# Optimization experiments

Hardware: AMD Instinct MI355X
Metric: run time of the kernel (lower is better)

The kernel has to match this reference:

```python
import jax, jax.numpy as jnp
import numpy as np

IN_DIM, DIM_MSA, PAIR_DIM = 256, 32, 64
B, L = 1, 512


def setup_inputs() -> dict:
    key = jax.random.key(0)
    k0, k1, k2, k3, k4 = jax.random.split(key, 5)
    seq_rep = jax.random.normal(k0, (B, L, IN_DIM), dtype=jnp.float32)
    # torch nn.Linear params: weight [out, in], bias [out]
    s1 = 1.0 / np.sqrt(IN_DIM)
    W1 = jax.random.uniform(k1, (DIM_MSA, IN_DIM), jnp.float32, -s1, s1)
    b1 = jax.random.uniform(k2, (DIM_MSA,), jnp.float32, -s1, s1)
    s2 = 1.0 / np.sqrt(DIM_MSA * DIM_MSA)
    W2 = jax.random.uniform(k3, (PAIR_DIM, DIM_MSA * DIM_MSA), jnp.float32, -s2, s2)
    b2 = jax.random.uniform(k4, (PAIR_DIM,), jnp.float32, -s2, s2)
    return {"seq_rep": seq_rep, "W1": W1, "b1": b1, "W2": W2, "b2": b2}


def reference(seq_rep, W1, b1, W2, b2):
    # proj_down1: [B,L,in_dim] -> [B,L,dim_msa]
    x = seq_rep @ W1.T + b1
    # outer product: 'bid,bjc -> bijcd' then flatten (c d)
    # [B,L(i),L(j),c(dim_msa),d(dim_msa)]
    outer = jnp.einsum('bid,bjc->bijcd', x, x)
    Bb, Li, Lj = outer.shape[:3]
    outer = outer.reshape(Bb, Li, Lj, DIM_MSA * DIM_MSA)  # (c d), c-major
    # proj_down2: -> [B,L,L,pairwise_dim]
    return outer @ W2.T + b2
```

## Files before the change

### kernel.cpp

```cpp
#include <hip/hip_runtime.h>


static constexpr int LL  = 512;
static constexpr int IND = 256;
static constexpr int DM  = 32;
static constexpr int PD  = 64;

typedef _Float16 f16x8 __attribute__((ext_vector_type(8)));
typedef float    f32x16 __attribute__((ext_vector_type(16)));

#define LGKM_BARRIER() do { \
    asm volatile("s_waitcnt lgkmcnt(0)" ::: "memory"); \
    __builtin_amdgcn_s_barrier(); \
  } while (0)

__global__ __launch_bounds__(256) void k_proj1(const float* __restrict__ seq,
                                               const float* __restrict__ W1,
                                               const float* __restrict__ b1,
                                               float* __restrict__ xg,
                                               _Float16* __restrict__ xgh) {
  __shared__ float part[8][DM];
  const int i   = blockIdx.x;
  const int t   = threadIdx.x;
  const int d   = t & 31;
  const int seg = t >> 5;
  const float* srow = seq + (size_t)i * IND + seg * 32;
  const float* wrow = W1  + (size_t)d * IND + seg * 32;
  float acc = 0.f;
#pragma unroll
  for (int k = 0; k < 32; k += 4) {
    const float4 s4 = *(const float4*)(srow + k);
    const float4 w4 = *(const float4*)(wrow + k);
    acc = fmaf(s4.x, w4.x, acc);
    acc = fmaf(s4.y, w4.y, acc);
    acc = fmaf(s4.z, w4.z, acc);
    acc = fmaf(s4.w, w4.w, acc);
  }
  part[seg][d] = acc;
  __syncthreads();
  if (t < DM) {
    float s = b1[t];
#pragma unroll
    for (int g = 0; g < 8; ++g) s += part[g][t];
    xg[i * DM + t]  = s;
    xgh[i * DM + t] = (_Float16)s;
  }
}

__global__ __launch_bounds__(256) void k_y(const float* __restrict__ xg,
                                           const float* __restrict__ W2,
                                           _Float16* __restrict__ Ygh) {
  __shared__ __align__(16) float xs[64][36];
  __shared__ __align__(16) float ws2[64][36];
  const int c     = blockIdx.x & 31;
  const int ibase = (blockIdx.x >> 5) * 64;
  const int t     = threadIdx.x;
#pragma unroll
  for (int k = 0; k < 2; ++k) {
    const int idx = t + k * 256;
    const int il = idx >> 3, d4 = idx & 7;
    const float4 v = *(const float4*)(xg + (size_t)(ibase + il) * DM + d4 * 4);
    *(float4*)&xs[il][d4 * 4] = v;
  }
#pragma unroll
  for (int k = 0; k < 2; ++k) {
    const int idx = t + k * 256;
    const int p = idx >> 3, d4 = idx & 7;
    const float4 v = *(const float4*)(W2 + (size_t)p * (DM * DM) + c * DM + d4 * 4);
    *(float4*)&ws2[p][d4 * 4] = v;
  }
  __syncthreads();
  const int p  = t & 63;
  const int ig = t >> 6;
  float wv[DM];
#pragma unroll
  for (int q = 0; q < 8; ++q) {
    const float4 v = *(const float4*)&ws2[p][q * 4];
    wv[q * 4 + 0] = v.x; wv[q * 4 + 1] = v.y;
    wv[q * 4 + 2] = v.z; wv[q * 4 + 3] = v.w;
  }
#pragma unroll
  for (int il = 0; il < 16; ++il) {
    const int row = ig * 16 + il;
    float a = 0.f;
#pragma unroll
    for (int q = 0; q < 8; ++q) {
      const float4 v = *(const float4*)&xs[row][q * 4];
      a = fmaf(wv[q * 4 + 0], v.x, a);
      a = fmaf(wv[q * 4 + 1], v.y, a);
      a = fmaf(wv[q * 4 + 2], v.z, a);
      a = fmaf(wv[q * 4 + 3], v.w, a);
    }
    Ygh[((size_t)(ibase + row) * DM + c) * PD + p] = (_Float16)a;
  }
}

static constexpr int XPAD = 40;

__global__ __launch_bounds__(128, 3) void k_outer(const _Float16* __restrict__ xgh,
                                                  const _Float16* __restrict__ Ygh,
                                                  const float* __restrict__ b2,
                                                  float* __restrict__ out) {
  __shared__ __align__(16) _Float16 xbs[128 * XPAD];
  __shared__ __align__(16) _Float16 ybs[2 * DM * PD];
  __shared__ __align__(16) float    obuf[2][32 * 32];
  const int q  = blockIdx.x & 3;
  const int i0 = blockIdx.x >> 2;
  const int t  = threadIdx.x;

  const int lane = t & 63;
  const int w    = t >> 6;
  const int l31  = lane & 31;
  const int lh   = lane >> 5;
  const int pn   = w * 32 + l31;
  float* const obufW = &obuf[w][0];
  const float4 bias4 = *(const float4*)(b2 + w * 32 + (lane & 7) * 4);

  {
    const f16x8* src = (const f16x8*)(xgh + (size_t)(q * 128 + t) * DM);
    _Float16* dst = &xbs[t * XPAD];
    *(f16x8*)(dst)      = src[0];
    *(f16x8*)(dst + 8)  = src[1];
    *(f16x8*)(dst + 16) = src[2];
    *(f16x8*)(dst + 24) = src[3];
  }
  {
    const f16x8* ys = (const f16x8*)(Ygh + (size_t)i0 * (DM * PD));
    *(f16x8*)&ybs[t * 8]        = ys[t];
    *(f16x8*)&ybs[1024 + t * 8] = ys[128 + t];
  }
  LGKM_BARRIER();

  const f16x8* ys1 = (const f16x8*)(Ygh + (size_t)(i0 + 256) * (DM * PD));
  const f16x8 n0 = ys1[t];
  const f16x8 n1 = ys1[128 + t];

  auto process = [&](int i, const _Float16* __restrict__ yb) {
    f16x8 b0, b1;
#pragma unroll
    for (int e = 0; e < 8; ++e) {
      b0[e] = yb[(lh * 8 + e) * PD + pn];
      b1[e] = yb[(16 + lh * 8 + e) * PD + pn];
    }
    const size_t orow0 = ((size_t)i * LL + q * 128) * PD;
#pragma unroll
    for (int jt = 0; jt < 4; ++jt) {
      const int ai = (jt * 32 + l31) * XPAD + lh * 8;
      const f16x8 a0 = *(const f16x8*)&xbs[ai];
      const f16x8 a1 = *(const f16x8*)&xbs[ai + 16];
      f32x16 acc = {};
      acc = __builtin_amdgcn_mfma_f32_32x32x16_f16(a0, b0, acc, 0, 0, 0);
      acc = __builtin_amdgcn_mfma_f32_32x32x16_f16(a1, b1, acc, 0, 0, 0);
#pragma unroll
      for (int r = 0; r < 16; ++r) {
        const int row = (r & 3) + 8 * (r >> 2) + 4 * lh;
        obufW[row * 32 + l31] = acc[r];
      }
#pragma unroll
      for (int k = 0; k < 4; ++k) {
        const int idx = lane + k * 64;
        const int row = idx >> 3, pseg = idx & 7;
        float4 v = *(const float4*)&obufW[idx * 4];
        v.x += bias4.x; v.y += bias4.y; v.z += bias4.z; v.w += bias4.w;
        *(float4*)(out + orow0 + (size_t)(jt * 32 + row) * PD + w * 32 + pseg * 4) = v;
      }
    }
  };

  process(i0, ybs);

  *(f16x8*)&ybs[2048 + t * 8]        = n0;
  *(f16x8*)&ybs[2048 + 1024 + t * 8] = n1;
  LGKM_BARRIER();

  process(i0 + 256, ybs + 2048);
}

extern "C" void kernel_launch(void* const* d_in, const int* in_sizes, int n_in,
                              void* d_out, int out_size, void* d_ws, size_t ws_size,
                              hipStream_t stream) {
  const float* seq = (const float*)d_in[0];
  const float* W1  = (const float*)d_in[1];
  const float* b1  = (const float*)d_in[2];
  const float* W2  = (const float*)d_in[3];
  const float* b2  = (const float*)d_in[4];
  float* out = (float*)d_out;

  float* xg     = (float*)d_ws;
  _Float16* xgh = (_Float16*)(xg + LL * DM);
  _Float16* Ygh = (_Float16*)(xg + LL * DM + LL * DM / 2);

  k_proj1<<<LL, 256, 0, stream>>>(seq, W1, b1, xg, xgh);
  k_y<<<256, 256, 0, stream>>>(xg, W2, Ygh);
  k_outer<<<LL * 2, 128, 0, stream>>>(xgh, Ygh, b2, out);
}
```

Measured before the change: 27.36 us.

## Fuse proj1 into Y kernel, computing x via fp16 MFMA per block

New measurement: 30.25 us. +10.5%, slower.

```diff
diff --git a/kernel.cpp b/kernel.cpp
--- a/kernel.cpp
+++ b/kernel.cpp
@@ -14,54 +14,29 @@
     __builtin_amdgcn_s_barrier(); \
   } while (0)
 
-__global__ __launch_bounds__(256) void k_proj1(const float* __restrict__ seq,
+__device__ __forceinline__ f16x8 cvt8(const float* __restrict__ p) {
+  const float4 a = *(const float4*)p;
+  const float4 b = *(const float4*)(p + 4);
+  f16x8 r;
+  r[0] = (_Float16)a.x; r[1] = (_Float16)a.y;
+  r[2] = (_Float16)a.z; r[3] = (_Float16)a.w;
+  r[4] = (_Float16)b.x; r[5] = (_Float16)b.y;
+  r[6] = (_Float16)b.z; r[7] = (_Float16)b.w;
+  return r;
+}
+
+__global__ __launch_bounds__(256) void k_front(const float* __restrict__ seq,
                                                const float* __restrict__ W1,
                                                const float* __restrict__ b1,
-                                               float* __restrict__ xg,
-                                               _Float16* __restrict__ xgh) {
-  __shared__ float part[8][DM];
-  const int i   = blockIdx.x;
-  const int t   = threadIdx.x;
-  const int d   = t & 31;
-  const int seg = t >> 5;
-  const float* srow = seq + (size_t)i * IND + seg * 32;
-  const float* wrow = W1  + (size_t)d * IND + seg * 32;
-  float acc = 0.f;
-#pragma unroll
-  for (int k = 0; k < 32; k += 4) {
-    const float4 s4 = *(const float4*)(srow + k);
-    const float4 w4 = *(const float4*)(wrow + k);
-    acc = fmaf(s4.x, w4.x, acc);
-    acc = fmaf(s4.y, w4.y, acc);
-    acc = fmaf(s4.z, w4.z, acc);
-    acc = fmaf(s4.w, w4.w, acc);
-  }
-  part[seg][d] = acc;
-  __syncthreads();
-  if (t < DM) {
-    float s = b1[t];
-#pragma unroll
-    for (int g = 0; g < 8; ++g) s += part[g][t];
-    xg[i * DM + t]  = s;
-    xgh[i * DM + t] = (_Float16)s;
-  }
-}
-
-__global__ __launch_bounds__(256) void k_y(const float* __restrict__ xg,
-                                           const float* __restrict__ W2,
-                                           _Float16* __restrict__ Ygh) {
+                                               const float* __restrict__ W2,
+                                               _Float16* __restrict__ xgh,
+                                               _Float16* __restrict__ Ygh) {
   __shared__ __align__(16) float xs[64][36];
   __shared__ __align__(16) float ws2[64][36];
   const int c     = blockIdx.x & 31;
   const int ibase = (blockIdx.x >> 5) * 64;
   const int t     = threadIdx.x;
-#pragma unroll
-  for (int k = 0; k < 2; ++k) {
-    const int idx = t + k * 256;
-    const int il = idx >> 3, d4 = idx & 7;
-    const float4 v = *(const float4*)(xg + (size_t)(ibase + il) * DM + d4 * 4);
-    *(float4*)&xs[il][d4 * 4] = v;
-  }
+
 #pragma unroll
   for (int k = 0; k < 2; ++k) {
     const int idx = t + k * 256;
@@ -69,29 +44,54 @@
     const float4 v = *(const float4*)(W2 + (size_t)p * (DM * DM) + c * DM + d4 * 4);
     *(float4*)&ws2[p][d4 * 4] = v;
   }
+
+  const int w = t >> 6, lane = t & 63, l31 = lane & 31, lh = lane >> 5;
+  if (w < 2) {
+    const int mbase = ibase + w * 32;
+    const float* arow = seq + (size_t)(mbase + l31) * IND + lh * 8;
+    const float* brow = W1  + (size_t)l31 * IND + lh * 8;
+    const float bias1 = b1[l31];
+    f32x16 acc = {};
+#pragma unroll
+    for (int ks = 0; ks < 16; ++ks) {
+      const f16x8 af = cvt8(arow + ks * 16);
+      const f16x8 bf = cvt8(brow + ks * 16);
+      acc = __builtin_amdgcn_mfma_f32_32x32x16_f16(af, bf, acc, 0, 0, 0);
+    }
+#pragma unroll
+    for (int r = 0; r < 16; ++r) {
+      const int mrow = (r & 3) + 8 * (r >> 2) + 4 * lh;
+      const float v = acc[r] + bias1;
+      xs[w * 32 + mrow][l31] = v;
+      if (c == 0) xgh[(size_t)(mbase + mrow) * DM + l31] = (_Float16)v;
+    }
+  }
   __syncthreads();
-  const int p  = t & 63;
-  const int ig = t >> 6;
-  float wv[DM];
-#pragma unroll
-  for (int q = 0; q < 8; ++q) {
-    const float4 v = *(const float4*)&ws2[p][q * 4];
-    wv[q * 4 + 0] = v.x; wv[q * 4 + 1] = v.y;
-    wv[q * 4 + 2] = v.z; wv[q * 4 + 3] = v.w;
-  }
-#pragma unroll
-  for (int il = 0; il < 16; ++il) {
-    const int row = ig * 16 + il;
-    float a = 0.f;
+
+  {
+    const int p  = t & 63;
+    const int ig = t >> 6;
+    float wv[DM];
 #pragma unroll
     for (int q = 0; q < 8; ++q) {
-      const float4 v = *(const float4*)&xs[row][q * 4];
-      a = fmaf(wv[q * 4 + 0], v.x, a);
-      a = fmaf(wv[q * 4 + 1], v.y, a);
-      a = fmaf(wv[q * 4 + 2], v.z, a);
-      a = fmaf(wv[q * 4 + 3], v.w, a);
+      const float4 v = *(const float4*)&ws2[p][q * 4];
+      wv[q * 4 + 0] = v.x; wv[q * 4 + 1] = v.y;
+      wv[q * 4 + 2] = v.z; wv[q * 4 + 3] = v.w;
     }
-    Ygh[((size_t)(ibase + row) * DM + c) * PD + p] = (_Float16)a;
+#pragma unroll
+    for (int il = 0; il < 16; ++il) {
+      const int row = ig * 16 + il;
+      float a = 0.f;
+#pragma unroll
+      for (int q = 0; q < 8; ++q) {
+        const float4 v = *(const float4*)&xs[row][q * 4];
+        a = fmaf(wv[q * 4 + 0], v.x, a);
+        a = fmaf(wv[q * 4 + 1], v.y, a);
+        a = fmaf(wv[q * 4 + 2], v.z, a);
+        a = fmaf(wv[q * 4 + 3], v.w, a);
+      }
+      Ygh[((size_t)(ibase + row) * DM + c) * PD + p] = (_Float16)a;
+    }
   }
 }
 
@@ -186,11 +186,9 @@
   const float* b2  = (const float*)d_in[4];
   float* out = (float*)d_out;
 
-  float* xg     = (float*)d_ws;
-  _Float16* xgh = (_Float16*)(xg + LL * DM);
-  _Float16* Ygh = (_Float16*)(xg + LL * DM + LL * DM / 2);
+  _Float16* xgh = (_Float16*)d_ws;
+  _Float16* Ygh = xgh + LL * DM;
 
-  k_proj1<<<LL, 256, 0, stream>>>(seq, W1, b1, xg, xgh);
-  k_y<<<256, 256, 0, stream>>>(xg, W2, Ygh);
+  k_front<<<256, 256, 0, stream>>>(seq, W1, b1, W2, xgh, Ygh);
   k_outer<<<LL * 2, 128, 0, stream>>>(xgh, Ygh, b2, out);
 }
```
